# Optimization experiments

Hardware: AMD Instinct MI355X
Metric: run time of the kernel (lower is better)

## Reference

```python
import jax, jax.numpy as jnp
import numpy as np
import math

SEQ_LEN = 2048
EMB = 1024
HEAD = 64
BATCH = 8

def setup_inputs() -> dict:
    key = jax.random.key(0)
    k1, k2, k3, k4 = jax.random.split(key, 4)
    x = jax.random.normal(k1, (BATCH, SEQ_LEN, EMB), dtype=jnp.float32)
    # torch Linear(no bias): out = x @ W.T with W [out,in]; store as [in,out]
    s = 1.0 / math.sqrt(EMB)
    Wk = jax.random.uniform(k2, (EMB, HEAD), dtype=jnp.float32, minval=-s, maxval=s)
    Wq = jax.random.uniform(k3, (EMB, HEAD), dtype=jnp.float32, minval=-s, maxval=s)
    Wv = jax.random.uniform(k4, (EMB, HEAD), dtype=jnp.float32, minval=-s, maxval=s)
    return {"x": x, "Wk": Wk, "Wq": Wq, "Wv": Wv}

def reference(x, Wk, Wq, Wv):
    B, S, E = x.shape
    H = Wk.shape[1]
    k = x @ Wk  # [B,S,H]
    q = x @ Wq
    v = x @ Wv
    scores = jnp.einsum('bsh,bth->bst', q, k) / math.sqrt(H)
    causal = jnp.tril(jnp.ones((S, S), dtype=bool))
    scores = jnp.where(causal[None], scores, -jnp.inf)
    attn = jax.nn.softmax(scores, axis=-1)
    # dropout is identity in eval mode
    return jnp.einsum('bst,bth->bsh', attn, v)
```

## Files before the change

### kernel.cpp

```cpp
#include <hip/hip_runtime.h>
#include <hip/hip_bf16.h>

typedef __attribute__((ext_vector_type(8))) short short8;
typedef __attribute__((ext_vector_type(4))) short short4v;
typedef __attribute__((ext_vector_type(4))) float floatx4;

#define SEQ   2048
#define EMB   1024
#define HEAD  64
#define BATCH 8

__device__ __forceinline__ short f2bf(float f) {
    union { float f; unsigned u; } a; a.f = f;
    unsigned u = a.u;
    u = (u + 0x7FFFu + ((u >> 16) & 1u)) >> 16;
    return (short)u;
}

__global__ void wtrans_kernel(const float* __restrict__ Wk,
                              const float* __restrict__ Wq,
                              const float* __restrict__ Wv,
                              short* __restrict__ Wf) {
    int gid  = blockIdx.x * 256 + threadIdx.x;
    int lane = gid & 63;
    int fid  = gid >> 6;
    int chunk = fid & 31;
    int mnt  = fid >> 5;
    int mat  = mnt >> 2, nt = mnt & 3;
    const float* src = (mat == 0) ? Wq : (mat == 1) ? Wk : Wv;
    int n = lane & 15, quad = lane >> 4;
    int h = nt * 16 + n;
    short8 o8;
    #pragma unroll
    for (int j = 0; j < 8; ++j) {
        int kk = chunk * 32 + quad * 8 + j;
        o8[j] = f2bf(src[kk * 64 + h]);
    }
    *(short8*)(Wf + (long)gid * 8) = o8;
}

__global__ __launch_bounds__(256) void qkv_kernel(const float* __restrict__ x,
                                                  const short* __restrict__ Wf,
                                                  short* __restrict__ q,
                                                  short* __restrict__ k,
                                                  short* __restrict__ vt) {
    __shared__ float red[3][64][48];
    const int wv   = threadIdx.x >> 6;
    const int lane = threadIdx.x & 63;
    const int l15  = lane & 15;
    const int quad = lane >> 4;
    const int row0 = blockIdx.x * 16;

    floatx4 acc[12];
    #pragma unroll
    for (int f = 0; f < 12; ++f) acc[f] = (floatx4){0.f, 0.f, 0.f, 0.f};

    const float* xrow = x + (long)(row0 + l15) * EMB + quad * 8;
    const int kbase = wv * 256;

    floatx4 xa = *(const floatx4*)(xrow + kbase);
    floatx4 xb = *(const floatx4*)(xrow + kbase + 4);

    #pragma unroll 1
    for (int kk = 0; kk < 256; kk += 32) {
        const int k0 = kbase + kk;
        short8 bfr[12];
        const short* wp = Wf + ((long)(k0 >> 5) * 64 + lane) * 8;
        #pragma unroll
        for (int f = 0; f < 12; ++f)
            bfr[f] = *(const short8*)(wp + (long)f * 32 * 64 * 8);
        const int kn = kbase + ((kk + 32) & 255);
        floatx4 na = *(const floatx4*)(xrow + kn);
        floatx4 nb = *(const floatx4*)(xrow + kn + 4);

        short8 a;
        #pragma unroll
        for (int i = 0; i < 4; ++i) { a[i] = f2bf(xa[i]); a[4 + i] = f2bf(xb[i]); }
        #pragma unroll
        for (int f = 0; f < 12; ++f)
            acc[f] = __builtin_amdgcn_mfma_f32_16x16x32_bf16(a, bfr[f], acc[f], 0, 0, 0);
        xa = na; xb = nb;
    }

    if (wv > 0) {
        #pragma unroll
        for (int f = 0; f < 12; ++f)
            #pragma unroll
            for (int r = 0; r < 4; ++r)
                red[wv - 1][lane][f * 4 + r] = acc[f][r];
    }
    __syncthreads();
    if (wv == 0) {
        #pragma unroll
        for (int w = 0; w < 3; ++w)
            #pragma unroll
            for (int f = 0; f < 12; ++f)
                #pragma unroll
                for (int r = 0; r < 4; ++r)
                    acc[f][r] += red[w][lane][f * 4 + r];

        const int bidx = row0 >> 11;
        const int srow = (row0 & (SEQ - 1)) + quad * 4;
        #pragma unroll
        for (int nt = 0; nt < 4; ++nt) {
            const int col = nt * 16 + l15;
            #pragma unroll
            for (int r = 0; r < 4; ++r) {
                long grow = (long)(row0 + quad * 4 + r);
                q[grow * HEAD + col] = f2bf(acc[nt][r]);
                k[grow * HEAD + col] = f2bf(acc[4 + nt][r]);
            }
            short4v vv;
            #pragma unroll
            for (int r = 0; r < 4; ++r) vv[r] = f2bf(acc[8 + nt][r]);
            *(short4v*)(vt + ((long)bidx * HEAD + col) * SEQ + srow) = vv;
        }
    }
}

__global__ __launch_bounds__(256) void attn_kernel(const short* __restrict__ q,
                                                   const short* __restrict__ k,
                                                   const short* __restrict__ vt,
                                                   float* __restrict__ out) {
    __shared__ short Plds[4][16][32];
    __shared__ float oA[4][16][64];
    __shared__ float lA[4][16];

    const int wv   = threadIdx.x >> 6;
    const int lane = threadIdx.x & 63;
    const int l15  = lane & 15;
    const int quad = lane >> 4;
    const int b    = blockIdx.x & 7;
    const int t    = 127 - (blockIdx.x >> 3);
    const int s0   = t * 16;

    const int nch  = (t + 2) >> 1;
    const int c0   = (nch * wv) >> 2;
    const int c1   = (nch * (wv + 1)) >> 2;
    const int cmax = (nch + 3) >> 2;

    const short* qb = q + ((long)b * SEQ + s0 + l15) * HEAD + quad * 8;
    short8 qf0 = *(const short8*)(qb);
    short8 qf1 = *(const short8*)(qb + 32);

    floatx4 o[4];
    #pragma unroll
    for (int nt = 0; nt < 4; ++nt) o[nt] = (floatx4){0.f, 0.f, 0.f, 0.f};
    float l_i[4] = {0.f, 0.f, 0.f, 0.f};

    for (int i = 0; i < cmax; ++i) {
        const int c = c0 + i;
        const bool act = (c < c1);
        const int j0 = c * 32;

        floatx4 sa[2];
        sa[0] = (floatx4){0.f, 0.f, 0.f, 0.f};
        sa[1] = (floatx4){0.f, 0.f, 0.f, 0.f};
        #pragma unroll
        for (int nt = 0; nt < 2; ++nt) {
            const short* kb = k + ((long)b * SEQ + j0 + nt * 16 + l15) * HEAD + quad * 8;
            short8 kf0 = *(const short8*)(kb);
            short8 kf1 = *(const short8*)(kb + 32);
            sa[nt] = __builtin_amdgcn_mfma_f32_16x16x32_bf16(qf0, kf0, sa[nt], 0, 0, 0);
            sa[nt] = __builtin_amdgcn_mfma_f32_16x16x32_bf16(qf1, kf1, sa[nt], 0, 0, 0);
        }

        #pragma unroll
        for (int r = 0; r < 4; ++r) {
            const int sq = s0 + quad * 4 + r;
            #pragma unroll
            for (int nt = 0; nt < 2; ++nt) {
                const int sk = j0 + nt * 16 + l15;
                float p = (!act || sk > sq) ? 0.f
                          : __expf(sa[nt][r] * 0.125f - 16.f);
                sa[nt][r] = p;
                l_i[r] += p;
            }
        }

        #pragma unroll
        for (int nt = 0; nt < 2; ++nt)
            #pragma unroll
            for (int r = 0; r < 4; ++r)
                Plds[wv][quad * 4 + r][nt * 16 + l15] = f2bf(sa[nt][r]);
        short8 pf = *(const short8*)(&Plds[wv][l15][quad * 8]);

        #pragma unroll
        for (int nt = 0; nt < 4; ++nt) {
            const short* vb = vt + ((long)b * HEAD + nt * 16 + l15) * SEQ + j0 + quad * 8;
            short8 vf = *(const short8*)(vb);
            o[nt] = __builtin_amdgcn_mfma_f32_16x16x32_bf16(pf, vf, o[nt], 0, 0, 0);
        }
    }

    #pragma unroll
    for (int msk = 1; msk <= 8; msk <<= 1) {
        #pragma unroll
        for (int r = 0; r < 4; ++r)
            l_i[r] += __shfl_xor(l_i[r], msk, 64);
    }
    if (l15 == 0) {
        #pragma unroll
        for (int r = 0; r < 4; ++r) lA[wv][quad * 4 + r] = l_i[r];
    }
    #pragma unroll
    for (int nt = 0; nt < 4; ++nt)
        #pragma unroll
        for (int r = 0; r < 4; ++r)
            oA[wv][quad * 4 + r][nt * 16 + l15] = o[nt][r];
    __syncthreads();

    {
        const int idx = threadIdx.x * 4;
        const int row = idx >> 6;
        const int col = idx & 63;
        const float l = lA[0][row] + lA[1][row] + lA[2][row] + lA[3][row];
        const float inv = 1.f / l;
        floatx4 ov;
        #pragma unroll
        for (int j = 0; j < 4; ++j)
            ov[j] = (oA[0][row][col + j] + oA[1][row][col + j]
                   + oA[2][row][col + j] + oA[3][row][col + j]) * inv;
        *(floatx4*)(out + ((long)b * SEQ + s0 + row) * HEAD + col) = ov;
    }
}

extern "C" void kernel_launch(void* const* d_in, const int* in_sizes, int n_in,
                              void* d_out, int out_size, void* d_ws, size_t ws_size,
                              hipStream_t stream) {
    const float* x  = (const float*)d_in[0];
    const float* Wk = (const float*)d_in[1];
    const float* Wq = (const float*)d_in[2];
    const float* Wv = (const float*)d_in[3];
    float* out = (float*)d_out;

    short* Wf = (short*)d_ws;
    short* q  = Wf + 3 * HEAD * EMB;
    short* k  = q + (long)BATCH * SEQ * HEAD;
    short* vt = k + (long)BATCH * SEQ * HEAD;

    hipLaunchKernelGGL(wtrans_kernel, dim3(96), dim3(256), 0, stream, Wk, Wq, Wv, Wf);
    hipLaunchKernelGGL(qkv_kernel, dim3(BATCH * SEQ / 16), dim3(256), 0, stream, x, Wf, q, k, vt);
    hipLaunchKernelGGL(attn_kernel, dim3(BATCH * 128), dim3(256), 0, stream, q, k, vt, out);
}
```

Measured before the change: 161.4 us.

## Prefetch next K/V chunk in attention loop and pad QKV reduction buffer

The attention kernel now software-pipelines its K and V fragment loads, issuing the next chunk's global loads before computing on the current chunk so memory latency overlaps MFMA and softmax work. The QKV kernel pads its shared reduction buffer to avoid LDS bank conflicts and simplifies weight address arithmetic. Both kernels gain a launch-bounds occupancy hint. The prefetch raises register pressure and adds a clamped redundant load on the last iteration.

After: 160.4 us. About the same (-0.6%).

```diff
diff --git a/kernel.cpp b/kernel.cpp
--- a/kernel.cpp
+++ b/kernel.cpp
@@ -39,12 +39,12 @@
     *(short8*)(Wf + (long)gid * 8) = o8;
 }
 
-__global__ __launch_bounds__(256) void qkv_kernel(const float* __restrict__ x,
-                                                  const short* __restrict__ Wf,
-                                                  short* __restrict__ q,
-                                                  short* __restrict__ k,
-                                                  short* __restrict__ vt) {
-    __shared__ float red[3][64][48];
+__global__ __launch_bounds__(256, 3) void qkv_kernel(const float* __restrict__ x,
+                                                     const short* __restrict__ Wf,
+                                                     short* __restrict__ q,
+                                                     short* __restrict__ k,
+                                                     short* __restrict__ vt) {
+    __shared__ float red[3][64][50];
     const int wv   = threadIdx.x >> 6;
     const int lane = threadIdx.x & 63;
     const int l15  = lane & 15;
@@ -56,6 +56,7 @@
     for (int f = 0; f < 12; ++f) acc[f] = (floatx4){0.f, 0.f, 0.f, 0.f};
 
     const float* xrow = x + (long)(row0 + l15) * EMB + quad * 8;
+    const short* wlane = Wf + (long)lane * 8;
     const int kbase = wv * 256;
 
     floatx4 xa = *(const floatx4*)(xrow + kbase);
@@ -63,12 +64,11 @@
 
     #pragma unroll 1
     for (int kk = 0; kk < 256; kk += 32) {
-        const int k0 = kbase + kk;
+        const int cidx = (kbase + kk) >> 5;
         short8 bfr[12];
-        const short* wp = Wf + ((long)(k0 >> 5) * 64 + lane) * 8;
         #pragma unroll
         for (int f = 0; f < 12; ++f)
-            bfr[f] = *(const short8*)(wp + (long)f * 32 * 64 * 8);
+            bfr[f] = *(const short8*)(wlane + (long)(f * 32 + cidx) * 512);
         const int kn = kbase + ((kk + 32) & 255);
         floatx4 na = *(const floatx4*)(xrow + kn);
         floatx4 nb = *(const floatx4*)(xrow + kn + 4);
@@ -118,10 +118,10 @@
     }
 }
 
-__global__ __launch_bounds__(256) void attn_kernel(const short* __restrict__ q,
-                                                   const short* __restrict__ k,
-                                                   const short* __restrict__ vt,
-                                                   float* __restrict__ out) {
+__global__ __launch_bounds__(256, 3) void attn_kernel(const short* __restrict__ q,
+                                                      const short* __restrict__ k,
+                                                      const short* __restrict__ vt,
+                                                      float* __restrict__ out) {
     __shared__ short Plds[4][16][32];
     __shared__ float oA[4][16][64];
     __shared__ float lA[4][16];
@@ -143,26 +143,54 @@
     short8 qf0 = *(const short8*)(qb);
     short8 qf1 = *(const short8*)(qb + 32);
 
+    const short* kbb = k + ((long)b * SEQ + l15) * HEAD + quad * 8;
+    const short* vbb = vt + ((long)b * HEAD + l15) * SEQ + quad * 8;
+
     floatx4 o[4];
     #pragma unroll
     for (int nt = 0; nt < 4; ++nt) o[nt] = (floatx4){0.f, 0.f, 0.f, 0.f};
     float l_i[4] = {0.f, 0.f, 0.f, 0.f};
 
+    short8 kf[2][2], vf[4];
+    {
+        const int j0 = c0 * 32;
+        #pragma unroll
+        for (int nt = 0; nt < 2; ++nt) {
+            const short* kb = kbb + (long)(j0 + nt * 16) * HEAD;
+            kf[nt][0] = *(const short8*)(kb);
+            kf[nt][1] = *(const short8*)(kb + 32);
+        }
+        #pragma unroll
+        for (int nt = 0; nt < 4; ++nt)
+            vf[nt] = *(const short8*)(vbb + (long)nt * 16 * SEQ + j0);
+    }
+
+    #pragma unroll 1
     for (int i = 0; i < cmax; ++i) {
         const int c = c0 + i;
         const bool act = (c < c1);
         const int j0 = c * 32;
 
+        const int cn = (c + 1 < nch) ? (c + 1) : (nch - 1);
+        const int jn = cn * 32;
+        short8 kn[2][2], vn[4];
+        #pragma unroll
+        for (int nt = 0; nt < 2; ++nt) {
+            const short* kb = kbb + (long)(jn + nt * 16) * HEAD;
+            kn[nt][0] = *(const short8*)(kb);
+            kn[nt][1] = *(const short8*)(kb + 32);
+        }
+        #pragma unroll
+        for (int nt = 0; nt < 4; ++nt)
+            vn[nt] = *(const short8*)(vbb + (long)nt * 16 * SEQ + jn);
+
         floatx4 sa[2];
         sa[0] = (floatx4){0.f, 0.f, 0.f, 0.f};
         sa[1] = (floatx4){0.f, 0.f, 0.f, 0.f};
         #pragma unroll
         for (int nt = 0; nt < 2; ++nt) {
-            const short* kb = k + ((long)b * SEQ + j0 + nt * 16 + l15) * HEAD + quad * 8;
-            short8 kf0 = *(const short8*)(kb);
-            short8 kf1 = *(const short8*)(kb + 32);
-            sa[nt] = __builtin_amdgcn_mfma_f32_16x16x32_bf16(qf0, kf0, sa[nt], 0, 0, 0);
-            sa[nt] = __builtin_amdgcn_mfma_f32_16x16x32_bf16(qf1, kf1, sa[nt], 0, 0, 0);
+            sa[nt] = __builtin_amdgcn_mfma_f32_16x16x32_bf16(qf0, kf[nt][0], sa[nt], 0, 0, 0);
+            sa[nt] = __builtin_amdgcn_mfma_f32_16x16x32_bf16(qf1, kf[nt][1], sa[nt], 0, 0, 0);
         }
 
         #pragma unroll
@@ -186,11 +214,13 @@
         short8 pf = *(const short8*)(&Plds[wv][l15][quad * 8]);
 
         #pragma unroll
-        for (int nt = 0; nt < 4; ++nt) {
-            const short* vb = vt + ((long)b * HEAD + nt * 16 + l15) * SEQ + j0 + quad * 8;
-            short8 vf = *(const short8*)(vb);
-            o[nt] = __builtin_amdgcn_mfma_f32_16x16x32_bf16(pf, vf, o[nt], 0, 0, 0);
-        }
+        for (int nt = 0; nt < 4; ++nt)
+            o[nt] = __builtin_amdgcn_mfma_f32_16x16x32_bf16(pf, vf[nt], o[nt], 0, 0, 0);
+
+        #pragma unroll
+        for (int nt = 0; nt < 2; ++nt) { kf[nt][0] = kn[nt][0]; kf[nt][1] = kn[nt][1]; }
+        #pragma unroll
+        for (int nt = 0; nt < 4; ++nt) vf[nt] = vn[nt];
     }
 
     #pragma unroll
```

## Fuse weight transform, QKV projection and attention into one cooperative kernel

Applied to the files above, without the earlier changes.

Replaces three separate kernel launches with a single cooperative kernel of 512 blocks that uses grid-wide syncs between the weight conversion, QKV projection and attention phases. The projection is re-split so each block handles 32 rows with a two-way K split instead of a four-way split. Attention pairs a short and a long causal tile per block to balance work. This removes launch gaps and tail effects, at the cost of grid.sync overhead and a constraint on occupancy (launch bounds of 2 blocks per CU).

Result: slower. 268.5 us (+66.4%).

```diff
diff --git a/kernel.cpp b/kernel.cpp
--- a/kernel.cpp
+++ b/kernel.cpp
@@ -1,5 +1,8 @@
 #include <hip/hip_runtime.h>
 #include <hip/hip_bf16.h>
+#include <hip/hip_cooperative_groups.h>
+
+namespace cg = cooperative_groups;
 
 typedef __attribute__((ext_vector_type(8))) short short8;
 typedef __attribute__((ext_vector_type(4))) short short4v;
@@ -17,211 +20,219 @@
     return (short)u;
 }
 
-__global__ void wtrans_kernel(const float* __restrict__ Wk,
-                              const float* __restrict__ Wq,
-                              const float* __restrict__ Wv,
-                              short* __restrict__ Wf) {
-    int gid  = blockIdx.x * 256 + threadIdx.x;
-    int lane = gid & 63;
-    int fid  = gid >> 6;
-    int chunk = fid & 31;
-    int mnt  = fid >> 5;
-    int mat  = mnt >> 2, nt = mnt & 3;
-    const float* src = (mat == 0) ? Wq : (mat == 1) ? Wk : Wv;
-    int n = lane & 15, quad = lane >> 4;
-    int h = nt * 16 + n;
-    short8 o8;
-    #pragma unroll
-    for (int j = 0; j < 8; ++j) {
-        int kk = chunk * 32 + quad * 8 + j;
-        o8[j] = f2bf(src[kk * 64 + h]);
-    }
-    *(short8*)(Wf + (long)gid * 8) = o8;
-}
-
-__global__ __launch_bounds__(256) void qkv_kernel(const float* __restrict__ x,
-                                                  const short* __restrict__ Wf,
-                                                  short* __restrict__ q,
-                                                  short* __restrict__ k,
-                                                  short* __restrict__ vt) {
-    __shared__ float red[3][64][48];
-    const int wv   = threadIdx.x >> 6;
-    const int lane = threadIdx.x & 63;
+__global__ __launch_bounds__(256, 2) void fused_kernel(
+        const float* __restrict__ x,  const float* __restrict__ Wk,
+        const float* __restrict__ Wq, const float* __restrict__ Wv,
+        float* __restrict__ out,      short* __restrict__ Wf,
+        short* __restrict__ q,        short* __restrict__ k,
+        short* __restrict__ vt) {
+    __shared__ __align__(16) char smem[25600];
+    cg::grid_group grid = cg::this_grid();
+
+    const int tid  = threadIdx.x;
+    const int bx   = blockIdx.x;
+    const int wv   = tid >> 6;
+    const int lane = tid & 63;
     const int l15  = lane & 15;
     const int quad = lane >> 4;
-    const int row0 = blockIdx.x * 16;
-
-    floatx4 acc[12];
-    #pragma unroll
-    for (int f = 0; f < 12; ++f) acc[f] = (floatx4){0.f, 0.f, 0.f, 0.f};
-
-    const float* xrow = x + (long)(row0 + l15) * EMB + quad * 8;
-    const int kbase = wv * 256;
-
-    floatx4 xa = *(const floatx4*)(xrow + kbase);
-    floatx4 xb = *(const floatx4*)(xrow + kbase + 4);
-
-    #pragma unroll 1
-    for (int kk = 0; kk < 256; kk += 32) {
-        const int k0 = kbase + kk;
-        short8 bfr[12];
-        const short* wp = Wf + ((long)(k0 >> 5) * 64 + lane) * 8;
+
+    {
+        int gid = bx * 256 + tid;
+        if (gid < 24576) {
+            int lane2 = gid & 63;
+            int fid   = gid >> 6;
+            int chunk = fid & 31;
+            int mnt   = fid >> 5;
+            int mat   = mnt >> 2, nt = mnt & 3;
+            const float* src = (mat == 0) ? Wq : (mat == 1) ? Wk : Wv;
+            int n = lane2 & 15, qd = lane2 >> 4;
+            int h = nt * 16 + n;
+            short8 o8;
+            #pragma unroll
+            for (int j = 0; j < 8; ++j)
+                o8[j] = f2bf(src[(chunk * 32 + qd * 8 + j) * 64 + h]);
+            *(short8*)(Wf + (long)gid * 8) = o8;
+        }
+    }
+    grid.sync();
+
+    {
+        float (*red)[64][50] = (float (*)[64][50])smem;
+        const int rowg  = (wv >> 1) * 16;
+        const int khalf = wv & 1;
+        const int row0  = bx * 32 + rowg;
+
+        floatx4 acc[12];
         #pragma unroll
-        for (int f = 0; f < 12; ++f)
-            bfr[f] = *(const short8*)(wp + (long)f * 32 * 64 * 8);
-        const int kn = kbase + ((kk + 32) & 255);
-        floatx4 na = *(const floatx4*)(xrow + kn);
-        floatx4 nb = *(const floatx4*)(xrow + kn + 4);
-
-        short8 a;
-        #pragma unroll
-        for (int i = 0; i < 4; ++i) { a[i] = f2bf(xa[i]); a[4 + i] = f2bf(xb[i]); }
-        #pragma unroll
-        for (int f = 0; f < 12; ++f)
-            acc[f] = __builtin_amdgcn_mfma_f32_16x16x32_bf16(a, bfr[f], acc[f], 0, 0, 0);
-        xa = na; xb = nb;
+        for (int f = 0; f < 12; ++f) acc[f] = (floatx4){0.f, 0.f, 0.f, 0.f};
+
+        const float* xrow  = x + (long)(row0 + l15) * EMB + quad * 8;
+        const short* wlane = Wf + (long)lane * 8;
+        const int kbase = khalf * 512;
+
+        floatx4 xa = *(const floatx4*)(xrow + kbase);
+        floatx4 xb = *(const floatx4*)(xrow + kbase + 4);
+
+        #pragma unroll 1
+        for (int kk = 0; kk < 512; kk += 32) {
+            const int cidx = (kbase + kk) >> 5;
+            short8 bfr[12];
+            #pragma unroll
+            for (int f = 0; f < 12; ++f)
+                bfr[f] = *(const short8*)(wlane + (long)(f * 32 + cidx) * 512);
+            const int kn = kbase + ((kk + 32) & 511);
+            floatx4 na = *(const floatx4*)(xrow + kn);
+            floatx4 nb = *(const floatx4*)(xrow + kn + 4);
+
+            short8 a;
+            #pragma unroll
+            for (int i = 0; i < 4; ++i) { a[i] = f2bf(xa[i]); a[4 + i] = f2bf(xb[i]); }
+            #pragma unroll
+            for (int f = 0; f < 12; ++f)
+                acc[f] = __builtin_amdgcn_mfma_f32_16x16x32_bf16(a, bfr[f], acc[f], 0, 0, 0);
+            xa = na; xb = nb;
+        }
+
+        if (khalf == 1) {
+            #pragma unroll
+            for (int f = 0; f < 12; ++f)
+                #pragma unroll
+                for (int r = 0; r < 4; ++r)
+                    red[wv >> 1][lane][f * 4 + r] = acc[f][r];
+        }
+        __syncthreads();
+        if (khalf == 0) {
+            #pragma unroll
+            for (int f = 0; f < 12; ++f)
+                #pragma unroll
+                for (int r = 0; r < 4; ++r)
+                    acc[f][r] += red[wv >> 1][lane][f * 4 + r];
+
+            const int bidx = row0 >> 11;
+            const int srow = (row0 & (SEQ - 1)) + quad * 4;
+            #pragma unroll
+            for (int nt = 0; nt < 4; ++nt) {
+                const int col = nt * 16 + l15;
+                #pragma unroll
+                for (int r = 0; r < 4; ++r) {
+                    long grow = (long)(row0 + quad * 4 + r);
+                    q[grow * HEAD + col] = f2bf(acc[nt][r]);
+                    k[grow * HEAD + col] = f2bf(acc[4 + nt][r]);
+                }
+                short4v vv;
+                #pragma unroll
+                for (int r = 0; r < 4; ++r) vv[r] = f2bf(acc[8 + nt][r]);
+                *(short4v*)(vt + ((long)bidx * HEAD + col) * SEQ + srow) = vv;
+            }
+        }
     }
-
-    if (wv > 0) {
-        #pragma unroll
-        for (int f = 0; f < 12; ++f)
-            #pragma unroll
-            for (int r = 0; r < 4; ++r)
-                red[wv - 1][lane][f * 4 + r] = acc[f][r];
-    }
-    __syncthreads();
-    if (wv == 0) {
-        #pragma unroll
-        for (int w = 0; w < 3; ++w)
-            #pragma unroll
-            for (int f = 0; f < 12; ++f)
-                #pragma unroll
-                for (int r = 0; r < 4; ++r)
-                    acc[f][r] += red[w][lane][f * 4 + r];
-
-        const int bidx = row0 >> 11;
-        const int srow = (row0 & (SEQ - 1)) + quad * 4;
-        #pragma unroll
-        for (int nt = 0; nt < 4; ++nt) {
-            const int col = nt * 16 + l15;
-            #pragma unroll
-            for (int r = 0; r < 4; ++r) {
-                long grow = (long)(row0 + quad * 4 + r);
-                q[grow * HEAD + col] = f2bf(acc[nt][r]);
-                k[grow * HEAD + col] = f2bf(acc[4 + nt][r]);
-            }
-            short4v vv;
-            #pragma unroll
-            for (int r = 0; r < 4; ++r) vv[r] = f2bf(acc[8 + nt][r]);
-            *(short4v*)(vt + ((long)bidx * HEAD + col) * SEQ + srow) = vv;
-        }
-    }
-}
-
-__global__ __launch_bounds__(256) void attn_kernel(const short* __restrict__ q,
-                                                   const short* __restrict__ k,
-                                                   const short* __restrict__ vt,
-                                                   float* __restrict__ out) {
-    __shared__ short Plds[4][16][32];
-    __shared__ float oA[4][16][64];
-    __shared__ float lA[4][16];
-
-    const int wv   = threadIdx.x >> 6;
-    const int lane = threadIdx.x & 63;
-    const int l15  = lane & 15;
-    const int quad = lane >> 4;
-    const int b    = blockIdx.x & 7;
-    const int t    = 127 - (blockIdx.x >> 3);
-    const int s0   = t * 16;
-
-    const int nch  = (t + 2) >> 1;
-    const int c0   = (nch * wv) >> 2;
-    const int c1   = (nch * (wv + 1)) >> 2;
-    const int cmax = (nch + 3) >> 2;
-
-    const short* qb = q + ((long)b * SEQ + s0 + l15) * HEAD + quad * 8;
-    short8 qf0 = *(const short8*)(qb);
-    short8 qf1 = *(const short8*)(qb + 32);
-
-    floatx4 o[4];
-    #pragma unroll
-    for (int nt = 0; nt < 4; ++nt) o[nt] = (floatx4){0.f, 0.f, 0.f, 0.f};
-    float l_i[4] = {0.f, 0.f, 0.f, 0.f};
-
-    for (int i = 0; i < cmax; ++i) {
-        const int c = c0 + i;
-        const bool act = (c < c1);
-        const int j0 = c * 32;
-
-        floatx4 sa[2];
-        sa[0] = (floatx4){0.f, 0.f, 0.f, 0.f};
-        sa[1] = (floatx4){0.f, 0.f, 0.f, 0.f};
-        #pragma unroll
-        for (int nt = 0; nt < 2; ++nt) {
-            const short* kb = k + ((long)b * SEQ + j0 + nt * 16 + l15) * HEAD + quad * 8;
-            short8 kf0 = *(const short8*)(kb);
-            short8 kf1 = *(const short8*)(kb + 32);
-            sa[nt] = __builtin_amdgcn_mfma_f32_16x16x32_bf16(qf0, kf0, sa[nt], 0, 0, 0);
-            sa[nt] = __builtin_amdgcn_mfma_f32_16x16x32_bf16(qf1, kf1, sa[nt], 0, 0, 0);
-        }
-
-        #pragma unroll
-        for (int r = 0; r < 4; ++r) {
-            const int sq = s0 + quad * 4 + r;
-            #pragma unroll
-            for (int nt = 0; nt < 2; ++nt) {
-                const int sk = j0 + nt * 16 + l15;
-                float p = (!act || sk > sq) ? 0.f
-                          : __expf(sa[nt][r] * 0.125f - 16.f);
-                sa[nt][r] = p;
-                l_i[r] += p;
-            }
-        }
-
-        #pragma unroll
-        for (int nt = 0; nt < 2; ++nt)
-            #pragma unroll
-            for (int r = 0; r < 4; ++r)
-                Plds[wv][quad * 4 + r][nt * 16 + l15] = f2bf(sa[nt][r]);
-        short8 pf = *(const short8*)(&Plds[wv][l15][quad * 8]);
-
-        #pragma unroll
-        for (int nt = 0; nt < 4; ++nt) {
-            const short* vb = vt + ((long)b * HEAD + nt * 16 + l15) * SEQ + j0 + quad * 8;
-            short8 vf = *(const short8*)(vb);
-            o[nt] = __builtin_amdgcn_mfma_f32_16x16x32_bf16(pf, vf, o[nt], 0, 0, 0);
-        }
-    }
-
-    #pragma unroll
-    for (int msk = 1; msk <= 8; msk <<= 1) {
-        #pragma unroll
-        for (int r = 0; r < 4; ++r)
-            l_i[r] += __shfl_xor(l_i[r], msk, 64);
-    }
-    if (l15 == 0) {
-        #pragma unroll
-        for (int r = 0; r < 4; ++r) lA[wv][quad * 4 + r] = l_i[r];
-    }
-    #pragma unroll
-    for (int nt = 0; nt < 4; ++nt)
-        #pragma unroll
-        for (int r = 0; r < 4; ++r)
-            oA[wv][quad * 4 + r][nt * 16 + l15] = o[nt][r];
-    __syncthreads();
+    grid.sync();
 
     {
-        const int idx = threadIdx.x * 4;
-        const int row = idx >> 6;
-        const int col = idx & 63;
-        const float l = lA[0][row] + lA[1][row] + lA[2][row] + lA[3][row];
-        const float inv = 1.f / l;
-        floatx4 ov;
-        #pragma unroll
-        for (int j = 0; j < 4; ++j)
-            ov[j] = (oA[0][row][col + j] + oA[1][row][col + j]
-                   + oA[2][row][col + j] + oA[3][row][col + j]) * inv;
-        *(floatx4*)(out + ((long)b * SEQ + s0 + row) * HEAD + col) = ov;
+        short (*Plds)[16][40] = (short (*)[16][40])smem;
+        float (*oA)[16][64]   = (float (*)[16][64])(smem + 5120);
+        float (*lA)[16]       = (float (*)[16])(smem + 21504);
+        const int b  = bx & 7;
+        const int pr = bx >> 3;
+
+        const short* kbb = k  + ((long)b * SEQ  + l15) * HEAD + quad * 8;
+        const short* vbb = vt + ((long)b * HEAD + l15) * SEQ  + quad * 8;
+
+        #pragma unroll 1
+        for (int wt = 0; wt < 2; ++wt) {
+            const int t  = wt ? (127 - pr) : pr;
+            const int s0 = t * 16;
+            const int nch  = (t + 2) >> 1;
+            const int c0   = (nch * wv) >> 2;
+            const int c1   = (nch * (wv + 1)) >> 2;
+            const int cmax = (nch + 3) >> 2;
+
+            const short* qb = q + ((long)b * SEQ + s0 + l15) * HEAD + quad * 8;
+            short8 qf0 = *(const short8*)(qb);
+            short8 qf1 = *(const short8*)(qb + 32);
+
+            floatx4 o[4];
+            #pragma unroll
+            for (int nt = 0; nt < 4; ++nt) o[nt] = (floatx4){0.f, 0.f, 0.f, 0.f};
+            float l_i[4] = {0.f, 0.f, 0.f, 0.f};
+
+            #pragma unroll 2
+            for (int i = 0; i < cmax; ++i) {
+                const int c = c0 + i;
+                const bool act = (c < c1);
+                const int j0 = c * 32;
+
+                floatx4 sa[2];
+                sa[0] = (floatx4){0.f, 0.f, 0.f, 0.f};
+                sa[1] = (floatx4){0.f, 0.f, 0.f, 0.f};
+                #pragma unroll
+                for (int nt = 0; nt < 2; ++nt) {
+                    const short* kb = kbb + (long)(j0 + nt * 16) * HEAD;
+                    short8 kf0 = *(const short8*)(kb);
+                    short8 kf1 = *(const short8*)(kb + 32);
+                    sa[nt] = __builtin_amdgcn_mfma_f32_16x16x32_bf16(qf0, kf0, sa[nt], 0, 0, 0);
+                    sa[nt] = __builtin_amdgcn_mfma_f32_16x16x32_bf16(qf1, kf1, sa[nt], 0, 0, 0);
+                }
+
+                #pragma unroll
+                for (int r = 0; r < 4; ++r) {
+                    const int sq = s0 + quad * 4 + r;
+                    #pragma unroll
+                    for (int nt = 0; nt < 2; ++nt) {
+                        const int sk = j0 + nt * 16 + l15;
+                        float p = (!act || sk > sq) ? 0.f
+                                  : __expf(sa[nt][r] * 0.125f - 16.f);
+                        sa[nt][r] = p;
+                        l_i[r] += p;
+                    }
+                }
+
+                #pragma unroll
+                for (int nt = 0; nt < 2; ++nt)
+                    #pragma unroll
+                    for (int r = 0; r < 4; ++r)
+                        Plds[wv][quad * 4 + r][nt * 16 + l15] = f2bf(sa[nt][r]);
+                short8 pf = *(const short8*)(&Plds[wv][l15][quad * 8]);
+
+                #pragma unroll
+                for (int nt = 0; nt < 4; ++nt) {
+                    short8 vf = *(const short8*)(vbb + (long)nt * 16 * SEQ + j0);
+                    o[nt] = __builtin_amdgcn_mfma_f32_16x16x32_bf16(pf, vf, o[nt], 0, 0, 0);
+                }
+            }
+
+            #pragma unroll
+            for (int msk = 1; msk <= 8; msk <<= 1) {
+                #pragma unroll
+                for (int r = 0; r < 4; ++r)
+                    l_i[r] += __shfl_xor(l_i[r], msk, 64);
+            }
+            if (l15 == 0) {
+                #pragma unroll
+                for (int r = 0; r < 4; ++r) lA[wv][quad * 4 + r] = l_i[r];
+            }
+            #pragma unroll
+            for (int nt = 0; nt < 4; ++nt)
+                #pragma unroll
+                for (int r = 0; r < 4; ++r)
+                    oA[wv][quad * 4 + r][nt * 16 + l15] = o[nt][r];
+            __syncthreads();
+
+            {
+                const int idx = tid * 4;
+                const int row = idx >> 6;
+                const int col = idx & 63;
+                const float l = lA[0][row] + lA[1][row] + lA[2][row] + lA[3][row];
+                const float inv = 1.f / l;
+                floatx4 ov;
+                #pragma unroll
+                for (int j = 0; j < 4; ++j)
+                    ov[j] = (oA[0][row][col + j] + oA[1][row][col + j]
+                           + oA[2][row][col + j] + oA[3][row][col + j]) * inv;
+                *(floatx4*)(out + ((long)b * SEQ + s0 + row) * HEAD + col) = ov;
+            }
+            __syncthreads();
+        }
     }
 }
 
@@ -239,7 +250,8 @@
     short* k  = q + (long)BATCH * SEQ * HEAD;
     short* vt = k + (long)BATCH * SEQ * HEAD;
 
-    hipLaunchKernelGGL(wtrans_kernel, dim3(96), dim3(256), 0, stream, Wk, Wq, Wv, Wf);
-    hipLaunchKernelGGL(qkv_kernel, dim3(BATCH * SEQ / 16), dim3(256), 0, stream, x, Wf, q, k, vt);
-    hipLaunchKernelGGL(attn_kernel, dim3(BATCH * 128), dim3(256), 0, stream, q, k, vt, out);
+    void* args[] = { (void*)&x, (void*)&Wk, (void*)&Wq, (void*)&Wv,
+                     (void*)&out, (void*)&Wf, (void*)&q, (void*)&k, (void*)&vt };
+    hipLaunchCooperativeKernel(fused_kernel, dim3(512), dim3(256),
+                               args, 0u, stream);
 }
```
